# Optimization experiments

Hardware: AMD Instinct MI355X
Metric: run time of the kernel (lower is better)

Reference implementation:

```python
import jax, jax.numpy as jnp
import numpy as np
import math

FREQS = jnp.array([1., 2., 4., 8., 7., 5.], dtype=jnp.float32)  # default frequencies


def setup_inputs() -> dict:
    key = jax.random.key(0)
    k1, k2, k3 = jax.random.split(key, 3)
    B, N, H, F = 8, 4096, 256, 6
    x = jax.random.normal(k1, (B, N, H), dtype=jnp.float32)
    t = jax.random.uniform(k2, (B, 1), dtype=jnp.float32) * (2.0 * math.pi)
    oscillators = jax.random.normal(k3, (F, H, H), dtype=jnp.float32) * 0.1
    # phase_shifts[i] = i / F * pi, broadcast over hidden dim (matches torch init)
    phase_shifts = jnp.broadcast_to(
        (jnp.arange(F, dtype=jnp.float32) / F * math.pi)[:, None], (F, H)
    ).copy()
    return {"x": x, "t": t, "oscillators": oscillators, "phase_shifts": phase_shifts}


def reference(x, t, oscillators, phase_shifts):
    # resonator[b, f, h] = sin(freq_f * t[b, 0] + phase[f, h])
    res = jnp.sin(FREQS[None, :, None] * t[:, :, None] + phase_shifts[None, :, :])  # [B, F, H]
    # result[b, n, k] = sum_f (x[b, n, :] @ W_f)[k] * res[b, f, k]
    return jnp.einsum('bnh,fhk,bfk->bnk', x, oscillators, res)
```

## Files before the change

kernel.cpp:

```cpp
#include <hip/hip_runtime.h>
#include <hip/hip_bf16.h>


#define B_  8
#define N_  4096
#define H_  256

typedef __attribute__((ext_vector_type(8))) short s8v;
typedef __attribute__((ext_vector_type(4))) float f4v;

#define AS1 __attribute__((address_space(1)))
#define AS3 __attribute__((address_space(3)))
#define GLOAD_LDS16(g, l) \
    __builtin_amdgcn_global_load_lds((const AS1 void*)(g), (AS3 void*)(l), 16, 0, 0)

__global__ __launch_bounds__(256) void build_w(
    const float* __restrict__ osc,
    const float* __restrict__ t,
    const float* __restrict__ phase,
    __hip_bfloat16* __restrict__ Wt)
{
    const float freqs[6] = {1.f, 2.f, 4.f, 8.f, 7.f, 5.f};
    __shared__ float tr[16 * 68];

    const int b  = blockIdx.z;
    const int n0 = blockIdx.y * 64;
    const int h0 = blockIdx.x * 16;
    const int tid = threadIdx.x;

    const float tb = t[b];
    const int nr = (tid & 15) * 4;
    const int hr = tid >> 4;
    float s[6][4];
#pragma unroll
    for (int f = 0; f < 6; ++f)
#pragma unroll
        for (int j = 0; j < 4; ++j)
            s[f][j] = __sinf(freqs[f] * tb + phase[f * 256 + n0 + nr + j]);

    const int h = h0 + hr;
    float4 acc = make_float4(0.f, 0.f, 0.f, 0.f);
#pragma unroll
    for (int f = 0; f < 6; ++f) {
        float4 o = *(const float4*)&osc[f * 65536 + h * 256 + n0 + nr];
        acc.x += o.x * s[f][0];
        acc.y += o.y * s[f][1];
        acc.z += o.z * s[f][2];
        acc.w += o.w * s[f][3];
    }
    *(float4*)&tr[hr * 68 + nr] = acc;
    __syncthreads();

    const int nw = tid >> 2;
    const int hw = (tid & 3) * 4;
    float v0 = tr[(hw + 0) * 68 + nw];
    float v1 = tr[(hw + 1) * 68 + nw];
    float v2 = tr[(hw + 2) * 68 + nw];
    float v3 = tr[(hw + 3) * 68 + nw];
    union { __hip_bfloat162 h2[2]; unsigned long long q; } cv;
    cv.h2[0] = __float22bfloat162_rn(make_float2(v0, v1));
    cv.h2[1] = __float22bfloat162_rn(make_float2(v2, v3));
    *(unsigned long long*)(Wt + (size_t)b * 65536 + (size_t)(n0 + nw) * 256 + h0 + hw) = cv.q;
}

#define LDA 72

__global__ __launch_bounds__(512, 4) void gemm(
    const float* __restrict__ X,
    const __hip_bfloat16* __restrict__ Wt,
    float* __restrict__ out)
{
    __shared__ short As[64 * LDA];
    __shared__ short Bs[2][256 * 64];

    const int b     = blockIdx.y;
    const int mTile = blockIdx.x;

    const int tid    = threadIdx.x;
    const int lane   = tid & 63;
    const int wave   = tid >> 6;
    const int lane15 = lane & 15;
    const int quad   = lane >> 4;
    const int wm     = wave >> 2;
    const int wn     = wave & 3;

    const float* Xb          = X   + (size_t)b * N_ * H_ + (size_t)mTile * 64 * H_;
    const __hip_bfloat16* Wb = Wt  + (size_t)b * H_ * H_;
    float* Ob                = out + (size_t)b * N_ * H_ + (size_t)mTile * 64 * H_;

    const int arow = tid >> 3;
    const int aseg = (tid & 7) * 8;
    const float* pa = Xb + (size_t)arow * H_ + aseg;

    const int brow = lane >> 3;
    const int bchk = (lane & 7) ^ brow;
    const __hip_bfloat16* pbg = Wb + (size_t)(wave * 32 + brow) * H_ + bchk * 8;

    f4v acc[2][4] = {};

#pragma unroll
    for (int j = 0; j < 4; ++j)
        GLOAD_LDS16(pbg + (size_t)j * 8 * H_, &Bs[0][wave * 2048 + j * 512]);
    float4 av[2][2];
    av[0][0] = *(const float4*)(pa + 0);
    av[0][1] = *(const float4*)(pa + 4);

#pragma unroll
    for (int it = 0; it < 4; ++it) {
        const int p = it & 1;
        union { __hip_bfloat162 h2[4]; uint4 q; } cv;
        cv.h2[0] = __float22bfloat162_rn(make_float2(av[p][0].x, av[p][0].y));
        cv.h2[1] = __float22bfloat162_rn(make_float2(av[p][0].z, av[p][0].w));
        cv.h2[2] = __float22bfloat162_rn(make_float2(av[p][1].x, av[p][1].y));
        cv.h2[3] = __float22bfloat162_rn(make_float2(av[p][1].z, av[p][1].w));
        *(uint4*)&As[arow * LDA + aseg] = cv.q;

        if (it < 3) {
#pragma unroll
            for (int j = 0; j < 4; ++j)
                GLOAD_LDS16(pbg + (it + 1) * 64 + (size_t)j * 8 * H_,
                            &Bs[p ^ 1][wave * 2048 + j * 512]);
            av[p ^ 1][0] = *(const float4*)(pa + (it + 1) * 64);
            av[p ^ 1][1] = *(const float4*)(pa + (it + 1) * 64 + 4);
            asm volatile("s_waitcnt vmcnt(6) lgkmcnt(0)\n\ts_barrier" ::: "memory");
        } else {
            asm volatile("s_waitcnt vmcnt(0) lgkmcnt(0)\n\ts_barrier" ::: "memory");
        }

#pragma unroll
        for (int kh = 0; kh < 2; ++kh) {
            s8v af[2], bf[4];
#pragma unroll
            for (int mt = 0; mt < 2; ++mt)
                af[mt] = *(const s8v*)&As[(wm * 32 + mt * 16 + lane15) * LDA + kh * 32 + quad * 8];
#pragma unroll
            for (int nt = 0; nt < 4; ++nt) {
                const int n  = wn * 64 + nt * 16 + lane15;
                const int pc = ((kh * 4 + quad) ^ (lane15 & 7)) * 8;
                bf[nt] = *(const s8v*)&Bs[p][n * 64 + pc];
            }
#pragma unroll
            for (int mt = 0; mt < 2; ++mt)
#pragma unroll
                for (int nt = 0; nt < 4; ++nt)
                    acc[mt][nt] = __builtin_amdgcn_mfma_f32_16x16x32_bf16(
                        af[mt], bf[nt], acc[mt][nt], 0, 0, 0);
        }
        if (it < 3)
            asm volatile("s_barrier" ::: "memory");
    }

#pragma unroll
    for (int mt = 0; mt < 2; ++mt) {
#pragma unroll
        for (int r = 0; r < 4; ++r) {
            int row = wm * 32 + mt * 16 + quad * 4 + r;
            float* po = Ob + (size_t)row * H_ + wn * 64 + lane15;
#pragma unroll
            for (int nt = 0; nt < 4; ++nt)
                __builtin_nontemporal_store(acc[mt][nt][r], po + nt * 16);
        }
    }
}

extern "C" void kernel_launch(void* const* d_in, const int* in_sizes, int n_in,
                              void* d_out, int out_size, void* d_ws, size_t ws_size,
                              hipStream_t stream) {
    const float* x     = (const float*)d_in[0];
    const float* t     = (const float*)d_in[1];
    const float* osc   = (const float*)d_in[2];
    const float* phase = (const float*)d_in[3];
    __hip_bfloat16* Wt = (__hip_bfloat16*)d_ws;
    float* out = (float*)d_out;
    (void)in_sizes; (void)n_in; (void)out_size; (void)ws_size;

    dim3 gw(16, 4, 8);
    build_w<<<gw, 256, 0, stream>>>(osc, t, phase, Wt);

    dim3 gg(64, 8);
    gemm<<<gg, 512, 0, stream>>>(x, Wt, out);
}
```

Measured before the change: 92.29 us.

## Preload all A tiles, prefetch B two stages ahead, vectorize output stores

The GEMM kernel now issues all four K-slices of the fp32 X tile as nontemporal loads up front instead of double-buffering them. B tiles are prefetched two stages ahead into the two LDS buffers, using a new swizzle pattern. The N-column mapping is permuted so each lane owns four consecutive output columns, which lets the epilogue write one 16-byte vector store per row instead of four scalar stores. The cost is more registers held for the A data and a more intricate wait-count and swizzle scheme that has to stay correct.

```diff
diff --git a/kernel.cpp b/kernel.cpp
--- a/kernel.cpp
+++ b/kernel.cpp
@@ -91,41 +91,46 @@
     const int arow = tid >> 3;
     const int aseg = (tid & 7) * 8;
     const float* pa = Xb + (size_t)arow * H_ + aseg;
+    f4v av[4][2];
+#pragma unroll
+    for (int it = 0; it < 4; ++it) {
+        av[it][0] = __builtin_nontemporal_load((const f4v*)(pa + it * 64));
+        av[it][1] = __builtin_nontemporal_load((const f4v*)(pa + it * 64 + 4));
+    }
 
     const int brow = lane >> 3;
-    const int bchk = (lane & 7) ^ brow;
-    const __hip_bfloat16* pbg = Wb + (size_t)(wave * 32 + brow) * H_ + bchk * 8;
+    const int bK   = lane >> 5;
+    const __hip_bfloat16* WbRow = Wb + (size_t)(wave * 32 + brow) * H_;
+
+#define ISSUE_B(buf, kt)                                                      \
+    do {                                                                      \
+        _Pragma("unroll")                                                     \
+        for (int j = 0; j < 4; ++j) {                                         \
+            const int csrc = (lane & 7) ^ (j * 2 + bK);                       \
+            GLOAD_LDS16(WbRow + (size_t)j * 8 * H_ + (kt) * 64 + csrc * 8,    \
+                        &Bs[buf][wave * 2048 + j * 512]);                     \
+        }                                                                     \
+    } while (0)
 
     f4v acc[2][4] = {};
 
-#pragma unroll
-    for (int j = 0; j < 4; ++j)
-        GLOAD_LDS16(pbg + (size_t)j * 8 * H_, &Bs[0][wave * 2048 + j * 512]);
-    float4 av[2][2];
-    av[0][0] = *(const float4*)(pa + 0);
-    av[0][1] = *(const float4*)(pa + 4);
+    ISSUE_B(0, 0);
+    ISSUE_B(1, 1);
 
 #pragma unroll
     for (int it = 0; it < 4; ++it) {
         const int p = it & 1;
         union { __hip_bfloat162 h2[4]; uint4 q; } cv;
-        cv.h2[0] = __float22bfloat162_rn(make_float2(av[p][0].x, av[p][0].y));
-        cv.h2[1] = __float22bfloat162_rn(make_float2(av[p][0].z, av[p][0].w));
-        cv.h2[2] = __float22bfloat162_rn(make_float2(av[p][1].x, av[p][1].y));
-        cv.h2[3] = __float22bfloat162_rn(make_float2(av[p][1].z, av[p][1].w));
+        cv.h2[0] = __float22bfloat162_rn(make_float2(av[it][0][0], av[it][0][1]));
+        cv.h2[1] = __float22bfloat162_rn(make_float2(av[it][0][2], av[it][0][3]));
+        cv.h2[2] = __float22bfloat162_rn(make_float2(av[it][1][0], av[it][1][1]));
+        cv.h2[3] = __float22bfloat162_rn(make_float2(av[it][1][2], av[it][1][3]));
         *(uint4*)&As[arow * LDA + aseg] = cv.q;
 
-        if (it < 3) {
-#pragma unroll
-            for (int j = 0; j < 4; ++j)
-                GLOAD_LDS16(pbg + (it + 1) * 64 + (size_t)j * 8 * H_,
-                            &Bs[p ^ 1][wave * 2048 + j * 512]);
-            av[p ^ 1][0] = *(const float4*)(pa + (it + 1) * 64);
-            av[p ^ 1][1] = *(const float4*)(pa + (it + 1) * 64 + 4);
-            asm volatile("s_waitcnt vmcnt(6) lgkmcnt(0)\n\ts_barrier" ::: "memory");
-        } else {
+        if (it < 3)
+            asm volatile("s_waitcnt vmcnt(4) lgkmcnt(0)\n\ts_barrier" ::: "memory");
+        else
             asm volatile("s_waitcnt vmcnt(0) lgkmcnt(0)\n\ts_barrier" ::: "memory");
-        }
 
 #pragma unroll
         for (int kh = 0; kh < 2; ++kh) {
@@ -135,7 +140,7 @@
                 af[mt] = *(const s8v*)&As[(wm * 32 + mt * 16 + lane15) * LDA + kh * 32 + quad * 8];
 #pragma unroll
             for (int nt = 0; nt < 4; ++nt) {
-                const int n  = wn * 64 + nt * 16 + lane15;
+                const int n  = wn * 64 + lane15 * 4 + nt;
                 const int pc = ((kh * 4 + quad) ^ (lane15 & 7)) * 8;
                 bf[nt] = *(const s8v*)&Bs[p][n * 64 + pc];
             }
@@ -146,19 +151,21 @@
                     acc[mt][nt] = __builtin_amdgcn_mfma_f32_16x16x32_bf16(
                         af[mt], bf[nt], acc[mt][nt], 0, 0, 0);
         }
-        if (it < 3)
+        if (it < 3) {
             asm volatile("s_barrier" ::: "memory");
+            if (it < 2)
+                ISSUE_B(p, it + 2);
+        }
     }
 
 #pragma unroll
     for (int mt = 0; mt < 2; ++mt) {
 #pragma unroll
         for (int r = 0; r < 4; ++r) {
-            int row = wm * 32 + mt * 16 + quad * 4 + r;
-            float* po = Ob + (size_t)row * H_ + wn * 64 + lane15;
-#pragma unroll
-            for (int nt = 0; nt < 4; ++nt)
-                __builtin_nontemporal_store(acc[mt][nt][r], po + nt * 16);
+            const int row = wm * 32 + mt * 16 + quad * 4 + r;
+            f4v o = { acc[mt][0][r], acc[mt][1][r], acc[mt][2][r], acc[mt][3][r] };
+            __builtin_nontemporal_store(o,
+                (f4v*)(Ob + (size_t)row * H_ + wn * 64 + lane15 * 4));
         }
     }
 }
```

New measurement: 96.96 us. 1.05x slower.
